# Kernel optimization log

Measured on AMD Instinct MI355X. Metric: run time of the kernel, lower is better.

## Reference

```python
import jax, jax.numpy as jnp
import numpy as np

B, CIN, COUT, H, W = 2, 256, 256, 96, 96
K, PAD, G = 3, 1, 4           # kernel, padding, deformable_groups
KK = K * K
CG = CIN // G                 # channels per deformable group


def setup_inputs() -> dict:
    key = jax.random.key(0)
    k1, k2, k3, k4 = jax.random.split(key, 4)
    feature = jax.random.normal(k1, (B, CIN, H, W), jnp.float32)
    pred_shape = jax.random.normal(k2, (B, H * W, 4), jnp.float32)
    # init_weights: normal(std=0.01), no biases
    w_offset = jax.random.normal(k3, (G * KK * 2, 4, 1, 1), jnp.float32) * 0.01
    w_deform = jax.random.normal(k4, (COUT, CIN, K, K), jnp.float32) * 0.01
    return {"feature": feature, "pred_shape": pred_shape,
            "w_offset": w_offset, "w_deform": w_deform}


def reference(feature, pred_shape, w_offset, w_deform):
    # pred_shape: (B, H*W, 4) -> (B, 4, H, W); detached in the original
    ps = jnp.transpose(pred_shape, (0, 2, 1)).reshape(B, -1, H, W)
    ps = jax.lax.stop_gradient(ps)
    # 1x1 offset conv: (B, G*2*KK, H, W)
    offset = jnp.einsum('bchw,oc->bohw', ps, w_offset[:, :, 0, 0])
    # mmcv layout per group: [y_k0, x_k0, y_k1, x_k1, ...]
    off = offset.reshape(B, G, KK, 2, H, W)
    off_y, off_x = off[:, :, :, 0], off[:, :, :, 1]   # (B, G, KK, H, W)

    kk = jnp.arange(KK)
    ky = (kk // K).reshape(KK, 1, 1).astype(jnp.float32)
    kx = (kk % K).reshape(KK, 1, 1).astype(jnp.float32)
    yy = jnp.arange(H, dtype=jnp.float32).reshape(1, H, 1)
    xx = jnp.arange(W, dtype=jnp.float32).reshape(1, 1, W)
    # sampling positions (stride=1, dilation=1): (B, G, KK, H, W)
    py = (yy - PAD + ky)[None, None] + off_y
    px = (xx - PAD + kx)[None, None] + off_x

    img = feature.reshape(B, G, CG, H * W)

    def gather(yi, xi):
        # zero outside the image (matches DCN bilinear with zero padding)
        valid = ((yi >= 0) & (yi < H) & (xi >= 0) & (xi < W)).astype(feature.dtype)
        idx = jnp.clip(yi, 0, H - 1) * W + jnp.clip(xi, 0, W - 1)
        v = jnp.take_along_axis(img, idx.reshape(B, G, 1, KK * H * W), axis=3)
        return v.reshape(B, G, CG, KK, H, W) * valid[:, :, None]

    y0 = jnp.floor(py); x0 = jnp.floor(px)
    ly = py - y0; lx = px - x0
    y0i = y0.astype(jnp.int32); x0i = x0.astype(jnp.int32)

    val = ((1 - ly) * (1 - lx))[:, :, None] * gather(y0i, x0i) \
        + ((1 - ly) * lx)[:, :, None] * gather(y0i, x0i + 1) \
        + (ly * (1 - lx))[:, :, None] * gather(y0i + 1, x0i) \
        + (ly * lx)[:, :, None] * gather(y0i + 1, x0i + 1)

    sampled = val.reshape(B, CIN, KK, H, W)
    out = jnp.einsum('bckhw,ock->bohw', sampled, w_deform.reshape(COUT, CIN, KK))
    return jax.nn.relu(out)
```

## Files before the change

kernel.cpp:

```cpp
#include <hip/hip_runtime.h>
#include <hip/hip_bf16.h>
#include <stdint.h>

#define HH   96
#define WW   96
#define HW   9216
#define CIN  256
#define COUT 256
#define NB   2
#define NG   4
#define CG   64
#define KK   9
#define KTOT 2304
#define KB   288
#define TS   8
#define WIN  12
#define SCH  32

typedef __attribute__((ext_vector_type(8))) short short8;
typedef __attribute__((ext_vector_type(4))) float f32x4;
typedef __attribute__((ext_vector_type(4))) uint32_t u32x4;

__device__ __forceinline__ uint32_t pk2bf(float v0, float v1) {
    __hip_bfloat162 h = __float22bfloat162_rn(make_float2(v0, v1));
    uint32_t u;
    __builtin_memcpy(&u, &h, 4);
    return u;
}

__global__ __launch_bounds__(256) void prep_A(const float* __restrict__ wd,
                                              uint16_t* __restrict__ Ablk) {
    int t  = blockIdx.x * 256 + threadIdx.x;
    int kb = t % KB;
    int o  = t / KB;
    int kkA = kb >> 5;
    int c0A = (kb & 31) * 8;
    const float* src = wd + (size_t)o * KTOT + c0A * KK + kkA;
    float a[8];
#pragma unroll
    for (int e = 0; e < 8; ++e) a[e] = src[e * KK];
    uint16_t* dst = Ablk + ((size_t)kb * 256 + o) * 8;
    u32x4 v;
    v.x = pk2bf(a[0], a[1]);
    v.y = pk2bf(a[2], a[3]);
    v.z = pk2bf(a[4], a[5]);
    v.w = pk2bf(a[6], a[7]);
    *(u32x4*)dst = v;
}

__global__ __launch_bounds__(256) void sampler(const float* __restrict__ feature,
                                               const float* __restrict__ pred,
                                               const float* __restrict__ woff,
                                               uint16_t* __restrict__ S) {
    __shared__ float ft[SCH * WIN * WIN];

    int tid = threadIdx.x;
    int cb = blockIdx.y, b = blockIdx.z;
    int ch0 = cb * SCH;
    int g = ch0 >> 6;
    int ty = blockIdx.x / (WW / TS), tx = blockIdx.x % (WW / TS);
    int r0 = ty * TS, c0 = tx * TS;
    int rlo = min(max(r0 - 2, 0), HH - WIN);
    int clo = min(max(c0 - 2, 0), WW - WIN);

    const float* fg = feature + ((size_t)(b * CIN + ch0)) * HW;
    for (int e = tid; e < SCH * WIN * WIN; e += 256) {
        int ch = e / (WIN * WIN);
        int re = e - ch * (WIN * WIN);
        int rr = re / WIN, cc = re - rr * WIN;
        ft[e] = fg[(size_t)ch * HW + (rlo + rr) * WW + clo + cc];
    }
    __syncthreads();

    int lane = tid & 63, wv = tid >> 6;
    int lr = lane >> 3, lc = lane & 7;
    int hy = r0 + lr, hx = c0 + lc;
    int p = hy * WW + hx;
    float4 ps4 = *(const float4*)(pred + ((size_t)b * HW + p) * 4);

    const float* ftw = ft + (wv * 8) * (WIN * WIN);
    const float* fgw = fg + (size_t)(wv * 8) * HW;
    int kb_base = cb * 4 + wv;

#pragma unroll
    for (int kk = 0; kk < KK; ++kk) {
        const float* wy = woff + (g * KK + kk) * 8;
        float offy = ps4.x * wy[0] + ps4.y * wy[1] + ps4.z * wy[2] + ps4.w * wy[3];
        float offx = ps4.x * wy[4] + ps4.y * wy[5] + ps4.z * wy[6] + ps4.w * wy[7];
        float py = (float)(hy - 1 + kk / 3) + offy;
        float px = (float)(hx - 1 + kk % 3) + offx;
        float fy = floorf(py), fx = floorf(px);
        int y0 = (int)fy, x0 = (int)fx;
        float ly = py - fy, lx = px - fx;
        int r = min(max(y0, 0), HH - 2);
        int q = min(max(x0, 0), WW - 2);
        float wyA = (y0 == r) ? (1.f - ly) : ((y0 == -1) ? ly : 0.f);
        float wyB = (y0 == r) ? ly : ((y0 == HH - 1) ? (1.f - ly) : 0.f);
        float wxA = (x0 == q) ? (1.f - lx) : ((x0 == -1) ? lx : 0.f);
        float wxB = (x0 == q) ? lx : ((x0 == WW - 1) ? (1.f - lx) : 0.f);
        float c00 = wyA * wxA, c01 = wyA * wxB;
        float c10 = wyB * wxA, c11 = wyB * wxB;

        bool fast = (r >= rlo) & (r <= rlo + WIN - 2) &
                    (q >= clo) & (q <= clo + WIN - 2);

        uint16_t* Sp = S + (((size_t)b * KB + (kk * 32 + kb_base)) * HW + p) * 8;
        uint32_t pk[4];

        if (fast) {
            int base = (r - rlo) * WIN + (q - clo);
#pragma unroll
            for (int ep = 0; ep < 4; ++ep) {
                const float* f0 = ftw + (2 * ep) * (WIN * WIN) + base;
                const float* f1 = f0 + (WIN * WIN);
                float v0 = c00 * f0[0] + c01 * f0[1] + c10 * f0[WIN] + c11 * f0[WIN + 1];
                float v1 = c00 * f1[0] + c01 * f1[1] + c10 * f1[WIN] + c11 * f1[WIN + 1];
                pk[ep] = pk2bf(v0, v1);
            }
        } else {
            size_t gb = (size_t)r * WW + q;
#pragma unroll
            for (int ep = 0; ep < 4; ++ep) {
                const float* f0 = fgw + (size_t)(2 * ep) * HW + gb;
                const float* f1 = f0 + HW;
                float v0 = c00 * f0[0] + c01 * f0[1] + c10 * f0[WW] + c11 * f0[WW + 1];
                float v1 = c00 * f1[0] + c01 * f1[1] + c10 * f1[WW] + c11 * f1[WW + 1];
                pk[ep] = pk2bf(v0, v1);
            }
        }
        u32x4 vv = {pk[0], pk[1], pk[2], pk[3]};
        *(u32x4*)(Sp) = vv;
    }
}

__global__ __launch_bounds__(64, 2) void gemm_kernel(const uint16_t* __restrict__ S,
                                                     const uint16_t* __restrict__ Ablk,
                                                     float* __restrict__ out) {
    int lane = threadIdx.x;
    int bid = blockIdx.x;
    int xcd = bid & 7;
    int j   = bid >> 3;
    int my  = j & 3;
    int pairid = xcd * 36 + (j >> 2);
    int b  = pairid / 144;
    int py = pairid % 144;
    int o0 = my * 64, col0 = py * 64;
    int kc = lane >> 4, il = lane & 15;

    const uint16_t* Ap = Ablk + ((size_t)kc * 256 + o0 + il) * 8;
    const uint16_t* Bp = S + (size_t)b * KB * HW * 8 + ((size_t)kc * HW + col0 + il) * 8;
    const size_t Astep = (size_t)4 * 256 * 8;
    const size_t Bstep = (size_t)4 * HW * 8;

    f32x4 acc[4][4];
#pragma unroll
    for (int m = 0; m < 4; ++m)
#pragma unroll
        for (int n = 0; n < 4; ++n) acc[m][n] = (f32x4){0.f, 0.f, 0.f, 0.f};

    const int NT = KTOT / 32;

    short8 a0[4], b0[4], a1[4], b1[4];

#define LOADT(t, areg, breg)                                                   \
    {                                                                          \
        const uint16_t* ap = Ap + (size_t)(t) * Astep;                         \
        const uint16_t* bp = Bp + (size_t)(t) * Bstep;                         \
        areg[0] = *(const short8*)(ap + 0 * 16 * 8);                           \
        areg[1] = *(const short8*)(ap + 1 * 16 * 8);                           \
        areg[2] = *(const short8*)(ap + 2 * 16 * 8);                           \
        areg[3] = *(const short8*)(ap + 3 * 16 * 8);                           \
        breg[0] = *(const short8*)(bp + 0 * 16 * 8);                           \
        breg[1] = *(const short8*)(bp + 1 * 16 * 8);                           \
        breg[2] = *(const short8*)(bp + 2 * 16 * 8);                           \
        breg[3] = *(const short8*)(bp + 3 * 16 * 8);                           \
    }

#define MFMAT(areg, breg)                                                      \
    {                                                                          \
        _Pragma("unroll")                                                      \
        for (int m = 0; m < 4; ++m)                                            \
            _Pragma("unroll")                                                  \
            for (int n = 0; n < 4; ++n)                                        \
                acc[m][n] = __builtin_amdgcn_mfma_f32_16x16x32_bf16(           \
                    areg[m], breg[n], acc[m][n], 0, 0, 0);                     \
    }

    LOADT(0, a0, b0);
    LOADT(1, a1, b1);

    for (int tt = 0; tt < NT; tt += 2) {
        MFMAT(a0, b0);
        if (tt + 2 < NT) LOADT(tt + 2, a0, b0);
        MFMAT(a1, b1);
        if (tt + 3 < NT) LOADT(tt + 3, a1, b1);
    }
#undef LOADT
#undef MFMAT

    int r4 = kc * 4;
    size_t obase = ((size_t)b * COUT + o0) * HW + col0;
#pragma unroll
    for (int m = 0; m < 4; ++m)
#pragma unroll
        for (int n = 0; n < 4; ++n)
#pragma unroll
            for (int r = 0; r < 4; ++r) {
                float v = acc[m][n][r];
                v = v > 0.f ? v : 0.f;
                out[obase + (size_t)(m * 16 + r4 + r) * HW + n * 16 + il] = v;
            }
}

extern "C" void kernel_launch(void* const* d_in, const int* in_sizes, int n_in,
                              void* d_out, int out_size, void* d_ws, size_t ws_size,
                              hipStream_t stream) {
    (void)in_sizes; (void)n_in; (void)out_size; (void)ws_size;
    const float* feature = (const float*)d_in[0];
    const float* pred    = (const float*)d_in[1];
    const float* woff    = (const float*)d_in[2];
    const float* wdef    = (const float*)d_in[3];
    float* out = (float*)d_out;

    const size_t S_BYTES = (size_t)NB * KB * HW * 8 * 2;
    uint16_t* S    = (uint16_t*)d_ws;
    uint16_t* Ablk = (uint16_t*)((char*)d_ws + S_BYTES);

    hipLaunchKernelGGL(prep_A, dim3(288), dim3(256), 0, stream, wdef, Ablk);
    hipLaunchKernelGGL(sampler, dim3((HH / TS) * (WW / TS), CIN / SCH, NB), dim3(256), 0, stream,
                       feature, pred, woff, S);
    hipLaunchKernelGGL(gemm_kernel, dim3(8 * (HW / 64) * NB / 8 * 4), dim3(64), 0, stream,
                       S, Ablk, out);
}
```

Baseline: 77.12 us.

## Pad sampler LDS tile, add interior fast path, deepen GEMM prefetch with 2-wave blocks

```diff
diff --git a/kernel.cpp b/kernel.cpp
--- a/kernel.cpp
+++ b/kernel.cpp
@@ -15,6 +15,7 @@
 #define KB   288
 #define TS   8
 #define WIN  12
+#define W2   13
 #define SCH  32
 
 typedef __attribute__((ext_vector_type(8))) short short8;
@@ -52,7 +53,7 @@
                                                const float* __restrict__ pred,
                                                const float* __restrict__ woff,
                                                uint16_t* __restrict__ S) {
-    __shared__ float ft[SCH * WIN * WIN];
+    __shared__ float ft[SCH * WIN * W2];
 
     int tid = threadIdx.x;
     int cb = blockIdx.y, b = blockIdx.z;
@@ -62,13 +63,16 @@
     int r0 = ty * TS, c0 = tx * TS;
     int rlo = min(max(r0 - 2, 0), HH - WIN);
     int clo = min(max(c0 - 2, 0), WW - WIN);
+    bool interior = (rlo >= 1) && (rlo + WIN <= HH - 1) &&
+                    (clo >= 1) && (clo + WIN <= WW - 1);
 
     const float* fg = feature + ((size_t)(b * CIN + ch0)) * HW;
     for (int e = tid; e < SCH * WIN * WIN; e += 256) {
         int ch = e / (WIN * WIN);
         int re = e - ch * (WIN * WIN);
         int rr = re / WIN, cc = re - rr * WIN;
-        ft[e] = fg[(size_t)ch * HW + (rlo + rr) * WW + clo + cc];
+        ft[ch * (WIN * W2) + rr * W2 + cc] =
+            fg[(size_t)ch * HW + (rlo + rr) * WW + clo + cc];
     }
     __syncthreads();
 
@@ -78,7 +82,7 @@
     int p = hy * WW + hx;
     float4 ps4 = *(const float4*)(pred + ((size_t)b * HW + p) * 4);
 
-    const float* ftw = ft + (wv * 8) * (WIN * WIN);
+    const float* ftw = ft + (wv * 8) * (WIN * W2);
     const float* fgw = fg + (size_t)(wv * 8) * HW;
     int kb_base = cb * 4 + wv;
 
@@ -92,40 +96,75 @@
         float fy = floorf(py), fx = floorf(px);
         int y0 = (int)fy, x0 = (int)fx;
         float ly = py - fy, lx = px - fx;
-        int r = min(max(y0, 0), HH - 2);
-        int q = min(max(x0, 0), WW - 2);
-        float wyA = (y0 == r) ? (1.f - ly) : ((y0 == -1) ? ly : 0.f);
-        float wyB = (y0 == r) ? ly : ((y0 == HH - 1) ? (1.f - ly) : 0.f);
-        float wxA = (x0 == q) ? (1.f - lx) : ((x0 == -1) ? lx : 0.f);
-        float wxB = (x0 == q) ? lx : ((x0 == WW - 1) ? (1.f - lx) : 0.f);
-        float c00 = wyA * wxA, c01 = wyA * wxB;
-        float c10 = wyB * wxA, c11 = wyB * wxB;
-
-        bool fast = (r >= rlo) & (r <= rlo + WIN - 2) &
-                    (q >= clo) & (q <= clo + WIN - 2);
 
         uint16_t* Sp = S + (((size_t)b * KB + (kk * 32 + kb_base)) * HW + p) * 8;
         uint32_t pk[4];
 
-        if (fast) {
-            int base = (r - rlo) * WIN + (q - clo);
-#pragma unroll
-            for (int ep = 0; ep < 4; ++ep) {
-                const float* f0 = ftw + (2 * ep) * (WIN * WIN) + base;
-                const float* f1 = f0 + (WIN * WIN);
-                float v0 = c00 * f0[0] + c01 * f0[1] + c10 * f0[WIN] + c11 * f0[WIN + 1];
-                float v1 = c00 * f1[0] + c01 * f1[1] + c10 * f1[WIN] + c11 * f1[WIN + 1];
-                pk[ep] = pk2bf(v0, v1);
+        if (interior) {
+            bool fast = (y0 >= rlo) & (y0 <= rlo + WIN - 2) &
+                        (x0 >= clo) & (x0 <= clo + WIN - 2);
+            if (fast) {
+                float c00 = (1.f - ly) * (1.f - lx), c01 = (1.f - ly) * lx;
+                float c10 = ly * (1.f - lx),         c11 = ly * lx;
+                int base = (y0 - rlo) * W2 + (x0 - clo);
+#pragma unroll
+                for (int ep = 0; ep < 4; ++ep) {
+                    const float* f0 = ftw + (2 * ep) * (WIN * W2) + base;
+                    const float* f1 = f0 + (WIN * W2);
+                    float v0 = c00 * f0[0] + c01 * f0[1] + c10 * f0[W2] + c11 * f0[W2 + 1];
+                    float v1 = c00 * f1[0] + c01 * f1[1] + c10 * f1[W2] + c11 * f1[W2 + 1];
+                    pk[ep] = pk2bf(v0, v1);
+                }
+            } else {
+                int r = min(max(y0, 0), HH - 2);
+                int q = min(max(x0, 0), WW - 2);
+                float wyA = (y0 == r) ? (1.f - ly) : ((y0 == -1) ? ly : 0.f);
+                float wyB = (y0 == r) ? ly : ((y0 == HH - 1) ? (1.f - ly) : 0.f);
+                float wxA = (x0 == q) ? (1.f - lx) : ((x0 == -1) ? lx : 0.f);
+                float wxB = (x0 == q) ? lx : ((x0 == WW - 1) ? (1.f - lx) : 0.f);
+                float c00 = wyA * wxA, c01 = wyA * wxB;
+                float c10 = wyB * wxA, c11 = wyB * wxB;
+                size_t gb = (size_t)r * WW + q;
+#pragma unroll
+                for (int ep = 0; ep < 4; ++ep) {
+                    const float* f0 = fgw + (size_t)(2 * ep) * HW + gb;
+                    const float* f1 = f0 + HW;
+                    float v0 = c00 * f0[0] + c01 * f0[1] + c10 * f0[WW] + c11 * f0[WW + 1];
+                    float v1 = c00 * f1[0] + c01 * f1[1] + c10 * f1[WW] + c11 * f1[WW + 1];
+                    pk[ep] = pk2bf(v0, v1);
+                }
             }
         } else {
-            size_t gb = (size_t)r * WW + q;
-#pragma unroll
-            for (int ep = 0; ep < 4; ++ep) {
-                const float* f0 = fgw + (size_t)(2 * ep) * HW + gb;
-                const float* f1 = f0 + HW;
-                float v0 = c00 * f0[0] + c01 * f0[1] + c10 * f0[WW] + c11 * f0[WW + 1];
-                float v1 = c00 * f1[0] + c01 * f1[1] + c10 * f1[WW] + c11 * f1[WW + 1];
-                pk[ep] = pk2bf(v0, v1);
+            int r = min(max(y0, 0), HH - 2);
+            int q = min(max(x0, 0), WW - 2);
+            float wyA = (y0 == r) ? (1.f - ly) : ((y0 == -1) ? ly : 0.f);
+            float wyB = (y0 == r) ? ly : ((y0 == HH - 1) ? (1.f - ly) : 0.f);
+            float wxA = (x0 == q) ? (1.f - lx) : ((x0 == -1) ? lx : 0.f);
+            float wxB = (x0 == q) ? lx : ((x0 == WW - 1) ? (1.f - lx) : 0.f);
+            float c00 = wyA * wxA, c01 = wyA * wxB;
+            float c10 = wyB * wxA, c11 = wyB * wxB;
+            bool fast = (r >= rlo) & (r <= rlo + WIN - 2) &
+                        (q >= clo) & (q <= clo + WIN - 2);
+            if (fast) {
+                int base = (r - rlo) * W2 + (q - clo);
+#pragma unroll
+                for (int ep = 0; ep < 4; ++ep) {
+                    const float* f0 = ftw + (2 * ep) * (WIN * W2) + base;
+                    const float* f1 = f0 + (WIN * W2);
+                    float v0 = c00 * f0[0] + c01 * f0[1] + c10 * f0[W2] + c11 * f0[W2 + 1];
+                    float v1 = c00 * f1[0] + c01 * f1[1] + c10 * f1[W2] + c11 * f1[W2 + 1];
+                    pk[ep] = pk2bf(v0, v1);
+                }
+            } else {
+                size_t gb = (size_t)r * WW + q;
+#pragma unroll
+                for (int ep = 0; ep < 4; ++ep) {
+                    const float* f0 = fgw + (size_t)(2 * ep) * HW + gb;
+                    const float* f1 = f0 + HW;
+                    float v0 = c00 * f0[0] + c01 * f0[1] + c10 * f0[WW] + c11 * f0[WW + 1];
+                    float v1 = c00 * f1[0] + c01 * f1[1] + c10 * f1[WW] + c11 * f1[WW + 1];
+                    pk[ep] = pk2bf(v0, v1);
+                }
             }
         }
         u32x4 vv = {pk[0], pk[1], pk[2], pk[3]};
@@ -133,18 +172,18 @@
     }
 }
 
-__global__ __launch_bounds__(64, 2) void gemm_kernel(const uint16_t* __restrict__ S,
-                                                     const uint16_t* __restrict__ Ablk,
-                                                     float* __restrict__ out) {
-    int lane = threadIdx.x;
-    int bid = blockIdx.x;
-    int xcd = bid & 7;
-    int j   = bid >> 3;
-    int my  = j & 3;
-    int pairid = xcd * 36 + (j >> 2);
-    int b  = pairid / 144;
-    int py = pairid % 144;
-    int o0 = my * 64, col0 = py * 64;
+__global__ __launch_bounds__(128, 2) void gemm_kernel(const uint16_t* __restrict__ S,
+                                                      const uint16_t* __restrict__ Ablk,
+                                                      float* __restrict__ out) {
+    int tid = threadIdx.x;
+    int lane = tid & 63, wv = tid >> 6;
+    int raw = blockIdx.x;
+    int wgid = (raw & 7) * 72 + (raw >> 3);
+    int b  = wgid / 288;
+    int rr = wgid % 288;
+    int py = rr >> 1, mp = rr & 1;
+    int o0 = (mp * 2 + wv) * 64;
+    int col0 = py * 64;
     int kc = lane >> 4, il = lane & 15;
 
     const uint16_t* Ap = Ablk + ((size_t)kc * 256 + o0 + il) * 8;
@@ -160,7 +199,7 @@
 
     const int NT = KTOT / 32;
 
-    short8 a0[4], b0[4], a1[4], b1[4];
+    short8 a0[4], b0[4], a1[4], b1[4], a2[4], b2[4], a3[4], b3[4];
 
 #define LOADT(t, areg, breg)                                                   \
     {                                                                          \
@@ -188,12 +227,18 @@
 
     LOADT(0, a0, b0);
     LOADT(1, a1, b1);
-
-    for (int tt = 0; tt < NT; tt += 2) {
+    LOADT(2, a2, b2);
+    LOADT(3, a3, b3);
+
+    for (int tt = 0; tt < NT; tt += 4) {
         MFMAT(a0, b0);
-        if (tt + 2 < NT) LOADT(tt + 2, a0, b0);
+        if (tt + 4 < NT) LOADT(tt + 4, a0, b0);
         MFMAT(a1, b1);
-        if (tt + 3 < NT) LOADT(tt + 3, a1, b1);
+        if (tt + 5 < NT) LOADT(tt + 5, a1, b1);
+        MFMAT(a2, b2);
+        if (tt + 6 < NT) LOADT(tt + 6, a2, b2);
+        MFMAT(a3, b3);
+        if (tt + 7 < NT) LOADT(tt + 7, a3, b3);
     }
 #undef LOADT
 #undef MFMAT
@@ -229,6 +274,6 @@
     hipLaunchKernelGGL(prep_A, dim3(288), dim3(256), 0, stream, wdef, Ablk);
     hipLaunchKernelGGL(sampler, dim3((HH / TS) * (WW / TS), CIN / SCH, NB), dim3(256), 0, stream,
                        feature, pred, woff, S);
-    hipLaunchKernelGGL(gemm_kernel, dim3(8 * (HW / 64) * NB / 8 * 4), dim3(64), 0, stream,
+    hipLaunchKernelGGL(gemm_kernel, dim3(576), dim3(128), 0, stream,
                        S, Ablk, out);
 }
```

After: 100.2 us. 1.3x slower.
